# Performance work log

Measured on AMD Instinct MI355X. Metric: run time of the kernel, lower is better.

## Reference

```python
import jax, jax.numpy as jnp
import numpy as np

VOCAB = 128000
SEED = 42
BATCH = 256
SEQ = 128
BIAS_FACTOR = 2.0
TOP_P = 0.9


def setup_inputs() -> dict:
    key = jax.random.key(0)
    k1, k2 = jax.random.split(key)
    input_ids = jax.random.randint(k1, (BATCH, SEQ), 0, VOCAB, dtype=jnp.int64 if jax.config.jax_enable_x64 else jnp.int32)
    scores = jax.random.normal(k2, (BATCH, VOCAB), dtype=jnp.float32) * 4.0
    # green list generated exactly as in the torch module: numpy rng, 0/1 per vocab entry
    green = jnp.asarray(np.random.default_rng(SEED).integers(0, 2, VOCAB), dtype=jnp.float32)
    return {"input_ids": input_ids, "scores": scores, "green": green}


def reference(input_ids, scores, green):
    B, V = scores.shape
    # bias green tokens, softmax over vocab
    logits = scores + BIAS_FACTOR * green[None, :]          # [B, V]
    probs = jax.nn.softmax(logits, axis=-1)                 # [B, V]
    # descending sort (torch.sort(descending=True))
    sorted_idx = jnp.argsort(-probs, axis=-1)               # [B, V]
    sorted_probs = jnp.take_along_axis(probs, sorted_idx, axis=-1)
    cum = jnp.cumsum(sorted_probs, axis=-1)                 # [B, V]
    # torch.searchsorted(cum, top_p, right=False): first i with cum[i] >= top_p
    cutoff = jnp.sum(cum < TOP_P, axis=-1, keepdims=True)   # [B, 1]
    # keep positions 0..cutoff inclusive (original zeroes cutoff+1:)
    keep = jnp.arange(V)[None, :] <= cutoff                 # [B, V]
    kept = jnp.where(keep, sorted_probs, 0.0)
    kept = kept / jnp.sum(kept, axis=-1, keepdims=True)
    kept = jnp.where(jnp.isfinite(kept), kept, 0.0)
    # multinomial(1) over truncated renormalized probs
    samp = jax.random.categorical(jax.random.key(1), jnp.log(kept), axis=-1)  # [B]
    next_tok = jnp.take_along_axis(sorted_idx, samp[:, None], axis=-1)[:, 0]  # [B]
    # scores[b,:] = 1e-5; scores[b, next_token] = 1e5
    out = jnp.full((B, V), 1e-5, dtype=scores.dtype)
    out = out.at[jnp.arange(B), next_tok].set(1e5)
    return out
```

## Files before the change

kernel.cpp:

```cpp
#include <hip/hip_runtime.h>
#include <cstdint>
#include <cstddef>

#define BATCH 256
#define VOCAB 128000
#define V4 (VOCAB/4)
#define NBINS 4096
#define CAP 4096
#define SPILLCAP 6144
#define GATE_HIST 1.0f
#define GATE_SPILL 8.0f
#define SPILL_BIN 3088u
#define M44 0xFFFFFFFFFFFull
#define FIX 16777216.0f
#define FIXINV 5.9604644775390625e-8f

__device__ __forceinline__ uint32_t rotl32(uint32_t v, int r){ return (v<<r)|(v>>(32-r)); }

__device__ __forceinline__ void threefry2x32_01(uint32_t& x0, uint32_t& x1){
  const uint32_t ks0=0u, ks1=1u, ks2=0x1BD11BDAu ^ 0u ^ 1u;
  x0+=ks0; x1+=ks1;
#define TF_R(r) { x0+=x1; x1=rotl32(x1,(r)); x1^=x0; }
  TF_R(13) TF_R(15) TF_R(26) TF_R(6)
  x0+=ks1; x1+=ks2+1u;
  TF_R(17) TF_R(29) TF_R(16) TF_R(24)
  x0+=ks2; x1+=ks0+2u;
  TF_R(13) TF_R(15) TF_R(26) TF_R(6)
  x0+=ks0; x1+=ks1+3u;
  TF_R(17) TF_R(29) TF_R(16) TF_R(24)
  x0+=ks1; x1+=ks2+4u;
  TF_R(13) TF_R(15) TF_R(26) TF_R(6)
  x0+=ks2; x1+=ks0+5u;
#undef TF_R
}

__device__ __forceinline__ float gumbel_at(uint32_t z){
  uint32_t x0 = 0u, x1 = z;
  threefry2x32_01(x0, x1);
  uint32_t bits = x0 ^ x1;
  uint32_t fb = (bits >> 9) | 0x3F800000u;
  float f = __uint_as_float(fb) - 1.0f;
  const float tiny = 1.17549435e-38f;
  float uu = fmaxf(tiny, f + tiny);
  return -logf(-logf(uu));
}

__device__ __forceinline__ uint32_t fkey(uint32_t u){
  return (u >> 31) ? ~u : (u | 0x80000000u);
}
__device__ __forceinline__ float pdecode(unsigned long long k){
  return __uint_as_float(~(uint32_t)(k >> 32));
}

__global__ __launch_bounds__(1024) void k_main(
    const float* __restrict__ scores, const float* __restrict__ green,
    float* __restrict__ out)
{
  __shared__ union {
    unsigned long long hist[NBINS];
    unsigned long long skeys[CAP];
  } u;
  __shared__ unsigned spill[SPILLCAP];
  __shared__ float red[1024];
  __shared__ unsigned long long wavewin[16];
  __shared__ unsigned n_sh, thr_sh, nsp_sh, fb_sh;
  __shared__ int cut_sh;

  const int b = blockIdx.x, tid = threadIdx.x;
  const int lane = tid & 63;
  const float4* row4 = (const float4*)(scores + (size_t)b * VOCAB);
  const float4* grn4 = (const float4*)green;
  float* orow = out + (size_t)b * VOCAB;
  float4* o4 = (float4*)orow;

  for (int i = tid; i < NBINS; i += 1024) u.hist[i] = 0ull;
  if (tid == 0) nsp_sh = 0u;
  __syncthreads();

  float lm = -INFINITY, ls16 = 0.f;
  const float4 fv = make_float4(1e-5f, 1e-5f, 1e-5f, 1e-5f);

#define PROC1(LV, II, CC) do { \
    float l_ = (LV); \
    lm = fmaxf(lm, l_); \
    float e_ = expf(l_ - 16.0f); \
    ls16 += e_; \
    if (l_ >= GATE_HIST){ \
      uint32_t bin_ = fkey(__float_as_uint(l_)) >> 20; \
      atomicAdd(&u.hist[bin_], (1ull<<44) | (unsigned long long)(unsigned)(e_ * FIX)); \
    } \
    bool pr_ = (l_ >= GATE_SPILL); \
    unsigned long long mk_ = __ballot(pr_); \
    if (pr_){ \
      unsigned off_ = (unsigned)__popcll(mk_ & ((1ull << lane) - 1ull)); \
      unsigned base_ = 0u; \
      if (off_ == 0u) base_ = atomicAdd(&nsp_sh, (unsigned)__popcll(mk_)); \
      base_ = (unsigned)__shfl((int)base_, (int)(__ffsll(mk_) - 1), 64); \
      unsigned pos_ = base_ + off_; \
      if (pos_ < SPILLCAP) spill[pos_] = (unsigned)(4*(II) + (CC)); \
    } \
  } while(0)

#define PROC4(SV, GV, II) do { \
    PROC1(fmaf(2.f, (GV).x, (SV).x), (II), 0); \
    PROC1(fmaf(2.f, (GV).y, (SV).y), (II), 1); \
    PROC1(fmaf(2.f, (GV).z, (SV).z), (II), 2); \
    PROC1(fmaf(2.f, (GV).w, (SV).w), (II), 3); \
  } while(0)

  for (int g7 = 0; g7 < 7; ++g7){
    const int i0 = tid + g7*4096, i1 = i0+1024, i2 = i0+2048, i3 = i0+3072;
    float4 sa = row4[i0], sb = row4[i1], sc = row4[i2], sd = row4[i3];
    float4 ga = grn4[i0], gb = grn4[i1], gc = grn4[i2], gd = grn4[i3];
    o4[i0] = fv; o4[i1] = fv; o4[i2] = fv; o4[i3] = fv;
    PROC4(sa, ga, i0); PROC4(sb, gb, i1); PROC4(sc, gc, i2); PROC4(sd, gd, i3);
  }
  {
    const int i0 = tid + 28672, i1 = i0+1024, i2 = i0+2048;
    float4 sa = row4[i0], sb = row4[i1], sc = row4[i2];
    float4 ga = grn4[i0], gb = grn4[i1], gc = grn4[i2];
    o4[i0] = fv; o4[i1] = fv; o4[i2] = fv;
    PROC4(sa, ga, i0); PROC4(sb, gb, i1); PROC4(sc, gc, i2);
  }
  if (tid < 256){
    const int i0 = tid + 31744;
    float4 sa = row4[i0];
    float4 ga = grn4[i0];
    o4[i0] = fv;
    PROC4(sa, ga, i0);
  }
#undef PROC4
#undef PROC1

  red[tid] = lm; __syncthreads();
  for (int s = 512; s > 0; s >>= 1){ if (tid < s) red[tid] = fmaxf(red[tid], red[tid+s]); __syncthreads(); }
  const float m = red[0];
  __syncthreads();
  red[tid] = ls16; __syncthreads();
  for (int s = 512; s > 0; s >>= 1){ if (tid < s) red[tid] += red[tid+s]; __syncthreads(); }
  const float S16 = red[0];
  __syncthreads();

  {
    float tm = 0.f;
    for (int i = tid; i < NBINS; i += 1024) tm += (float)(u.hist[i] & M44);
    red[tid] = tm * FIXINV;
  }
  __syncthreads();
  for (int s = 512; s > 0; s >>= 1){ if (tid < s) red[tid] += red[tid+s]; __syncthreads(); }
  if (tid == 0){
    float target = 0.903f * red[0];
    int top = (int)(fkey(__float_as_uint(m)) >> 20);
    float acc = 0.f; unsigned c = 0; unsigned result = (unsigned)top;
    for (int bin = top; bin >= 0; --bin){
      unsigned long long h = u.hist[bin];
      unsigned cb = (unsigned)(h >> 44);
      if (c + cb > CAP) break;
      acc += (float)(h & M44) * FIXINV; c += cb; result = (unsigned)bin;
      if (acc >= target){
        if (bin > 0 && c + (unsigned)(u.hist[bin-1] >> 44) <= CAP)
          result = (unsigned)(bin-1);
        break;
      }
    }
    thr_sh = result; n_sh = 0u;
    fb_sh = (nsp_sh > SPILLCAP || result < SPILL_BIN) ? 1u : 0u;
  }
  __syncthreads();
  const unsigned thr = thr_sh;

  if (!fb_sh){
    const unsigned nsp = nsp_sh;
    for (unsigned j = tid; j < nsp; j += 1024){
      unsigned idx = spill[j];
      float s = scores[(size_t)b * VOCAB + idx];
      float g = green[idx];
      float l = fmaf(2.f, g, s);
      if ((fkey(__float_as_uint(l)) >> 20) >= thr){
        unsigned pos = atomicAdd(&n_sh, 1u);
        float p = expf(l - 16.0f) / S16;
        if (pos < CAP)
          u.skeys[pos] = ((unsigned long long)(~__float_as_uint(p)) << 32) | idx;
      }
    }
  } else {
    for (int i = tid; i < V4; i += 1024){
      float4 s = row4[i], g = grn4[i];
      #pragma unroll
      for (int c = 0; c < 4; ++c){
        float l = fmaf(2.f, (&g.x)[c], (&s.x)[c]);
        if ((fkey(__float_as_uint(l)) >> 20) >= thr){
          unsigned pos = atomicAdd(&n_sh, 1u);
          float p = expf(l - 16.0f) / S16;
          if (pos < CAP)
            u.skeys[pos] = ((unsigned long long)(~__float_as_uint(p)) << 32) | (unsigned)(4*i + c);
        }
      }
    }
  }
  __syncthreads();
  unsigned n = n_sh; if (n > CAP) n = CAP;

  unsigned N2 = 2; while (N2 < n) N2 <<= 1;
  for (unsigned i = n + tid; i < N2; i += 1024) u.skeys[i] = 0xFFFFFFFFFFFFFFFFull;
  __syncthreads();
  for (unsigned k = 2; k <= N2; k <<= 1){
    for (unsigned j = k >> 1; j > 0; j >>= 1){
      for (unsigned i = tid; i < N2; i += 1024){
        unsigned ixj = i ^ j;
        if (ixj > i){
          unsigned long long a = u.skeys[i], c2 = u.skeys[ixj];
          bool up = ((i & k) == 0u);
          if ((a > c2) == up){ u.skeys[i] = c2; u.skeys[ixj] = a; }
        }
      }
      __syncthreads();
    }
  }

  unsigned C = (n + 1023) >> 10;
  {
    unsigned lo = tid * C; if (lo > n) lo = n;
    unsigned hi = lo + C;  if (hi > n) hi = n;
    float s = 0.f;
    for (unsigned j = lo; j < hi; ++j) s += pdecode(u.skeys[j]);
    red[tid] = s;
  }
  __syncthreads();
  if (tid == 0){
    float run = 0.f; int cut = (int)n - 1; int t = 0;
    for (; t < 1024; ++t){ float cs = red[t]; if (run + cs >= 0.9f) break; run += cs; }
    if (t < 1024){
      float c2 = run;
      for (unsigned j = (unsigned)t * C; j < n; ++j){
        c2 += pdecode(u.skeys[j]);
        if (c2 >= 0.9f){ cut = (int)j; break; }
      }
    }
    cut_sh = cut;
  }
  __syncthreads();
  const int cut = cut_sh;

  float best = -INFINITY; unsigned bj = 0x7FFFFFFFu;
  for (int j = tid; j <= cut; j += 1024){
    float p = pdecode(u.skeys[j]);
    float sc = logf(p) + gumbel_at((uint32_t)b * (uint32_t)VOCAB + (uint32_t)j);
    if (sc > best || (sc == best && (unsigned)j < bj)){ best = sc; bj = (unsigned)j; }
  }
  for (int off = 32; off > 0; off >>= 1){
    float osc = __shfl_down(best, off, 64);
    unsigned oj = __shfl_down(bj, off, 64);
    if (osc > best || (osc == best && oj < bj)){ best = osc; bj = oj; }
  }
  if ((tid & 63) == 0){
    uint32_t ub = __float_as_uint(best);
    uint32_t ou = (ub >> 31) ? ~ub : (ub | 0x80000000u);
    wavewin[tid >> 6] = ((unsigned long long)ou << 32) |
                        (unsigned long long)(0xFFFFFFFFu - bj);
  }
  __syncthreads();
  if (tid == 0){
    unsigned long long bb = 0ull;
    for (int w = 0; w < 16; ++w){ unsigned long long x = wavewin[w]; if (x > bb) bb = x; }
    unsigned jwin = 0xFFFFFFFFu - (unsigned)(bb & 0xFFFFFFFFull);
    orow[(size_t)(u.skeys[jwin] & 0xFFFFFFFFull)] = 1e5f;
  }
}

extern "C" void kernel_launch(void* const* d_in, const int* in_sizes, int n_in,
                              void* d_out, int out_size, void* d_ws, size_t ws_size,
                              hipStream_t stream) {
  const float* scores = (const float*)d_in[1];
  const float* green  = (const float*)d_in[2];
  float* out = (float*)d_out;
  (void)d_ws; (void)ws_size;

  hipLaunchKernelGGL(k_main, dim3(BATCH), dim3(1024), 0, stream, scores, green, out);
}
```

Baseline: 325.8 us.

## Split row processing into streaming kernel over quarter-rows plus per-row selection kernel

The single per-row kernel becomes three launches. A zero kernel clears counters. A streaming kernel splits each row into four 256-thread blocks that compute the partial max and exp-sum, write the fill value and spill candidate indices to global workspace through a global atomic counter. A per-row kernel then builds the histogram only from the spilled candidates and runs the existing threshold, sort and sample steps. The aim is better occupancy and bandwidth during the full-vocab pass and removal of per-element shared histogram atomics, at the cost of extra launches, global atomics and a workspace round trip. The histogram target now uses the total exp-sum instead of the sum over gated bins.

```diff
diff --git a/kernel.cpp b/kernel.cpp
--- a/kernel.cpp
+++ b/kernel.cpp
@@ -8,7 +8,6 @@
 #define NBINS 4096
 #define CAP 4096
 #define SPILLCAP 6144
-#define GATE_HIST 1.0f
 #define GATE_SPILL 8.0f
 #define SPILL_BIN 3088u
 #define M44 0xFFFFFFFFFFFull
@@ -52,104 +51,127 @@
   return __uint_as_float(~(uint32_t)(k >> 32));
 }
 
-__global__ __launch_bounds__(1024) void k_main(
+__global__ void k_zero(unsigned* __restrict__ cnt){
+  if (threadIdx.x < BATCH) cnt[threadIdx.x] = 0u;
+}
+
+__global__ __launch_bounds__(256) void k_stream(
     const float* __restrict__ scores, const float* __restrict__ green,
-    float* __restrict__ out)
+    float* __restrict__ out, unsigned* __restrict__ cnt,
+    float* __restrict__ pmax, float* __restrict__ psum,
+    unsigned* __restrict__ spill)
 {
-  __shared__ union {
-    unsigned long long hist[NBINS];
-    unsigned long long skeys[CAP];
-  } u;
-  __shared__ unsigned spill[SPILLCAP];
-  __shared__ float red[1024];
-  __shared__ unsigned long long wavewin[16];
-  __shared__ unsigned n_sh, thr_sh, nsp_sh, fb_sh;
-  __shared__ int cut_sh;
-
-  const int b = blockIdx.x, tid = threadIdx.x;
-  const int lane = tid & 63;
+  __shared__ float red[256];
+
+  const int blk = blockIdx.x;
+  const int b = blk >> 2, q = blk & 3;
+  const int tid = threadIdx.x, lane = tid & 63;
+  const int base = q * 8000;
   const float4* row4 = (const float4*)(scores + (size_t)b * VOCAB);
   const float4* grn4 = (const float4*)green;
-  float* orow = out + (size_t)b * VOCAB;
-  float4* o4 = (float4*)orow;
-
-  for (int i = tid; i < NBINS; i += 1024) u.hist[i] = 0ull;
-  if (tid == 0) nsp_sh = 0u;
-  __syncthreads();
+  float4* o4 = (float4*)(out + (size_t)b * VOCAB);
+  unsigned* sp_row = spill + (size_t)b * SPILLCAP;
+  const float4 fv = make_float4(1e-5f, 1e-5f, 1e-5f, 1e-5f);
 
   float lm = -INFINITY, ls16 = 0.f;
-  const float4 fv = make_float4(1e-5f, 1e-5f, 1e-5f, 1e-5f);
-
-#define PROC1(LV, II, CC) do { \
+
+#define SPILL1(LV, IDX) do { \
     float l_ = (LV); \
     lm = fmaxf(lm, l_); \
-    float e_ = expf(l_ - 16.0f); \
-    ls16 += e_; \
-    if (l_ >= GATE_HIST){ \
-      uint32_t bin_ = fkey(__float_as_uint(l_)) >> 20; \
-      atomicAdd(&u.hist[bin_], (1ull<<44) | (unsigned long long)(unsigned)(e_ * FIX)); \
-    } \
+    ls16 += expf(l_ - 16.0f); \
     bool pr_ = (l_ >= GATE_SPILL); \
     unsigned long long mk_ = __ballot(pr_); \
     if (pr_){ \
       unsigned off_ = (unsigned)__popcll(mk_ & ((1ull << lane) - 1ull)); \
       unsigned base_ = 0u; \
-      if (off_ == 0u) base_ = atomicAdd(&nsp_sh, (unsigned)__popcll(mk_)); \
+      if (off_ == 0u) base_ = atomicAdd(&cnt[b], (unsigned)__popcll(mk_)); \
       base_ = (unsigned)__shfl((int)base_, (int)(__ffsll(mk_) - 1), 64); \
       unsigned pos_ = base_ + off_; \
-      if (pos_ < SPILLCAP) spill[pos_] = (unsigned)(4*(II) + (CC)); \
+      if (pos_ < SPILLCAP) sp_row[pos_] = (IDX); \
     } \
   } while(0)
 
-#define PROC4(SV, GV, II) do { \
-    PROC1(fmaf(2.f, (GV).x, (SV).x), (II), 0); \
-    PROC1(fmaf(2.f, (GV).y, (SV).y), (II), 1); \
-    PROC1(fmaf(2.f, (GV).z, (SV).z), (II), 2); \
-    PROC1(fmaf(2.f, (GV).w, (SV).w), (II), 3); \
+#define SPROC4(SV, GV, II) do { \
+    SPILL1(fmaf(2.f, (GV).x, (SV).x), (unsigned)(4*(II)+0)); \
+    SPILL1(fmaf(2.f, (GV).y, (SV).y), (unsigned)(4*(II)+1)); \
+    SPILL1(fmaf(2.f, (GV).z, (SV).z), (unsigned)(4*(II)+2)); \
+    SPILL1(fmaf(2.f, (GV).w, (SV).w), (unsigned)(4*(II)+3)); \
   } while(0)
 
   for (int g7 = 0; g7 < 7; ++g7){
-    const int i0 = tid + g7*4096, i1 = i0+1024, i2 = i0+2048, i3 = i0+3072;
+    const int i0 = base + tid + g7*1024, i1 = i0+256, i2 = i0+512, i3 = i0+768;
     float4 sa = row4[i0], sb = row4[i1], sc = row4[i2], sd = row4[i3];
     float4 ga = grn4[i0], gb = grn4[i1], gc = grn4[i2], gd = grn4[i3];
     o4[i0] = fv; o4[i1] = fv; o4[i2] = fv; o4[i3] = fv;
-    PROC4(sa, ga, i0); PROC4(sb, gb, i1); PROC4(sc, gc, i2); PROC4(sd, gd, i3);
+    SPROC4(sa, ga, i0); SPROC4(sb, gb, i1); SPROC4(sc, gc, i2); SPROC4(sd, gd, i3);
   }
   {
-    const int i0 = tid + 28672, i1 = i0+1024, i2 = i0+2048;
+    const int i0 = base + 7168 + tid, i1 = i0+256, i2 = i0+512;
     float4 sa = row4[i0], sb = row4[i1], sc = row4[i2];
     float4 ga = grn4[i0], gb = grn4[i1], gc = grn4[i2];
     o4[i0] = fv; o4[i1] = fv; o4[i2] = fv;
-    PROC4(sa, ga, i0); PROC4(sb, gb, i1); PROC4(sc, gc, i2);
-  }
-  if (tid < 256){
-    const int i0 = tid + 31744;
+    SPROC4(sa, ga, i0); SPROC4(sb, gb, i1); SPROC4(sc, gc, i2);
+  }
+  if (tid < 64){
+    const int i0 = base + 7936 + tid;
     float4 sa = row4[i0];
     float4 ga = grn4[i0];
     o4[i0] = fv;
-    PROC4(sa, ga, i0);
-  }
-#undef PROC4
-#undef PROC1
+    SPROC4(sa, ga, i0);
+  }
+#undef SPROC4
+#undef SPILL1
 
   red[tid] = lm; __syncthreads();
-  for (int s = 512; s > 0; s >>= 1){ if (tid < s) red[tid] = fmaxf(red[tid], red[tid+s]); __syncthreads(); }
-  const float m = red[0];
+  for (int s = 128; s > 0; s >>= 1){ if (tid < s) red[tid] = fmaxf(red[tid], red[tid+s]); __syncthreads(); }
+  if (tid == 0) pmax[b*4 + q] = red[0];
   __syncthreads();
   red[tid] = ls16; __syncthreads();
-  for (int s = 512; s > 0; s >>= 1){ if (tid < s) red[tid] += red[tid+s]; __syncthreads(); }
-  const float S16 = red[0];
-  __syncthreads();
-
-  {
-    float tm = 0.f;
-    for (int i = tid; i < NBINS; i += 1024) tm += (float)(u.hist[i] & M44);
-    red[tid] = tm * FIXINV;
-  }
-  __syncthreads();
-  for (int s = 512; s > 0; s >>= 1){ if (tid < s) red[tid] += red[tid+s]; __syncthreads(); }
+  for (int s = 128; s > 0; s >>= 1){ if (tid < s) red[tid] += red[tid+s]; __syncthreads(); }
+  if (tid == 0) psum[b*4 + q] = red[0];
+}
+
+__global__ __launch_bounds__(1024) void k_row(
+    const float* __restrict__ scores, const float* __restrict__ green,
+    float* __restrict__ out, const unsigned* __restrict__ cnt,
+    const float* __restrict__ pmax, const float* __restrict__ psum,
+    const unsigned* __restrict__ spill)
+{
+  __shared__ unsigned long long sp64[SPILLCAP];
+  __shared__ union {
+    unsigned long long hist[NBINS];
+    unsigned long long skeys[CAP];
+  } u;
+  __shared__ float red[1024];
+  __shared__ unsigned long long wavewin[16];
+  __shared__ unsigned n_sh, thr_sh, fb_sh;
+  __shared__ int cut_sh;
+
+  const int b = blockIdx.x, tid = threadIdx.x;
+  const float* srow = scores + (size_t)b * VOCAB;
+  float* orow = out + (size_t)b * VOCAB;
+
+  const float m = fmaxf(fmaxf(pmax[b*4+0], pmax[b*4+1]), fmaxf(pmax[b*4+2], pmax[b*4+3]));
+  const float S16 = ((psum[b*4+0] + psum[b*4+1]) + psum[b*4+2]) + psum[b*4+3];
+  const unsigned nsp_total = cnt[b];
+  const unsigned nsp = nsp_total > SPILLCAP ? SPILLCAP : nsp_total;
+
+  for (int i = tid; i < NBINS; i += 1024) u.hist[i] = 0ull;
+  if (tid == 0) n_sh = 0u;
+  __syncthreads();
+
+  for (unsigned j = tid; j < nsp; j += 1024){
+    unsigned idx = spill[(size_t)b * SPILLCAP + j];
+    float l = fmaf(2.f, green[idx], srow[idx]);
+    sp64[j] = ((unsigned long long)__float_as_uint(l) << 32) | idx;
+    uint32_t bin = fkey(__float_as_uint(l)) >> 20;
+    atomicAdd(&u.hist[bin],
+              (1ull << 44) | (unsigned long long)(expf(l - 16.0f) * FIX));
+  }
+  __syncthreads();
+
   if (tid == 0){
-    float target = 0.903f * red[0];
+    float target = 0.903f * S16;
     int top = (int)(fkey(__float_as_uint(m)) >> 20);
     float acc = 0.f; unsigned c = 0; unsigned result = (unsigned)top;
     for (int bin = top; bin >= 0; --bin){
@@ -163,27 +185,26 @@
         break;
       }
     }
-    thr_sh = result; n_sh = 0u;
-    fb_sh = (nsp_sh > SPILLCAP || result < SPILL_BIN) ? 1u : 0u;
+    thr_sh = result;
+    fb_sh = (nsp_total > SPILLCAP || result < SPILL_BIN) ? 1u : 0u;
   }
   __syncthreads();
   const unsigned thr = thr_sh;
 
   if (!fb_sh){
-    const unsigned nsp = nsp_sh;
     for (unsigned j = tid; j < nsp; j += 1024){
-      unsigned idx = spill[j];
-      float s = scores[(size_t)b * VOCAB + idx];
-      float g = green[idx];
-      float l = fmaf(2.f, g, s);
-      if ((fkey(__float_as_uint(l)) >> 20) >= thr){
+      unsigned long long k = sp64[j];
+      uint32_t lb = (uint32_t)(k >> 32);
+      if ((fkey(lb) >> 20) >= thr){
         unsigned pos = atomicAdd(&n_sh, 1u);
-        float p = expf(l - 16.0f) / S16;
+        float p = expf(__uint_as_float(lb) - 16.0f) / S16;
         if (pos < CAP)
-          u.skeys[pos] = ((unsigned long long)(~__float_as_uint(p)) << 32) | idx;
+          u.skeys[pos] = ((unsigned long long)(~__float_as_uint(p)) << 32) | (k & 0xFFFFFFFFull);
       }
     }
   } else {
+    const float4* row4 = (const float4*)srow;
+    const float4* grn4 = (const float4*)green;
     for (int i = tid; i < V4; i += 1024){
       float4 s = row4[i], g = grn4[i];
       #pragma unroll
@@ -274,7 +295,14 @@
   const float* scores = (const float*)d_in[1];
   const float* green  = (const float*)d_in[2];
   float* out = (float*)d_out;
-  (void)d_ws; (void)ws_size;
-
-  hipLaunchKernelGGL(k_main, dim3(BATCH), dim3(1024), 0, stream, scores, green, out);
-}
+
+  unsigned* cnt = (unsigned*)d_ws;
+  float* pmax = (float*)d_ws + 256;
+  float* psum = pmax + 1024;
+  unsigned* spill = (unsigned*)(psum + 1024);
+  (void)ws_size;
+
+  hipLaunchKernelGGL(k_zero,   dim3(1),       dim3(256),  0, stream, cnt);
+  hipLaunchKernelGGL(k_stream, dim3(BATCH*4), dim3(256),  0, stream, scores, green, out, cnt, pmax, psum, spill);
+  hipLaunchKernelGGL(k_row,    dim3(BATCH),   dim3(1024), 0, stream, scores, green, out, cnt, pmax, psum, spill);
+}
```

After: 852.0 us. +161.5%, slower.
